# Kernel optimization log

Hardware: AMD Instinct MI355X
Metric: run time of the kernel (lower is better)

The kernel has to match this reference:

```python
import jax, jax.numpy as jnp
import numpy as np

THRESHOLD = 0.5
EPS = 1e-6


def setup_inputs() -> dict:
    key = jax.random.key(0)
    k1, k2 = jax.random.split(key)
    points = jax.random.normal(k1, (16, 10, 30, 2), dtype=jnp.float32)
    polys = jax.random.normal(k2, (16, 16, 200, 2), dtype=jnp.float32)
    return {"points": points, "drivable_multipolygon": polys}


def reference(points, drivable_multipolygon):
    # points: (B, C, T, 2); drivable_multipolygon: (B, K, N, 2)
    # Broadcast layout: (B, K, C, T, N-1, ...)
    ps = drivable_multipolygon[:, :, None, None, :-1, :]   # edge starts (B,K,1,1,N-1,2)
    pe = drivable_multipolygon[:, :, None, None, 1:, :]    # edge ends   (B,K,1,1,N-1,2)
    pts = points[:, None, :, :, None, :]                   # (B,1,C,T,1,2)

    # --- point-to-segment distance ---
    v1 = pts - ps
    ev = pe - ps
    dot = jnp.sum(v1 * ev, axis=-1)
    esq = jnp.sum(ev * ev, axis=-1)
    proj = jnp.clip(dot / (esq + EPS), 0.0, 1.0)
    closest = ev * proj[..., None] + ps
    dist_sq = jnp.maximum(jnp.sum((pts - closest) ** 2, axis=-1), EPS)
    min_dist = jnp.min(jnp.sqrt(dist_sq), axis=-1)         # min over edges N-1 -> (B,K,C,T)
    min_dist = jnp.min(min_dist, axis=1)                   # min over polygons K -> (B,C,T)

    # --- ray-casting inside test (parity of crossings) ---
    py = pts[..., 1]
    px = pts[..., 0]
    sy, sx = ps[..., 1], ps[..., 0]
    ey, ex = pe[..., 1], pe[..., 0]
    cond_y = ((sy <= py) & (py < ey)) | ((ey <= py) & (py < sy))
    slope = (ey - sy) / (ex - sx + EPS)
    intersect_x = sx + (py - sy) / (slope + EPS)
    is_left = intersect_x > px
    intersection = cond_y & is_left                        # (B,K,C,T,N-1)
    crossings = jnp.sum(jnp.sum(intersection.astype(jnp.int32), axis=-1), axis=1)  # (B,C,T)
    inside = (crossings % 2) == 1

    min_dist = jnp.where(inside, -min_dist, min_dist)
    min_dist = jax.nn.relu(min_dist + THRESHOLD)
    return jnp.sum(min_dist, axis=-1)                      # (B, C)
```

## Files before the change

kernel.cpp:

```cpp
#include <hip/hip_runtime.h>
#include <math.h>
#include <float.h>

#define EPS 1e-6f
#define THRESHOLD 0.5f

#define NB 16
#define NPOLY 16
#define NVERT 200
#define NSEG_PER_POLY 199
#define NSEG (NPOLY * NSEG_PER_POLY)
#define NPTB 300
#define HPTB 150
#define NPOINTS 4800
#define NSLICE 64
#define SEG_PER_SLICE 50


struct Seg { float sx, sy, evx, evy, inv_esq, errS, inv_slope, ey; };

__global__ __launch_bounds__(192) void seg_kernel(
    const float* __restrict__ points,
    const float* __restrict__ polys,
    float2* __restrict__ part,
    float* __restrict__ out)
{
    __shared__ float4 lds[SEG_PER_SLICE * 2];

    const int slice = blockIdx.x;
    const int b     = blockIdx.y;
    const int lp    = threadIdx.x;

    const int s0 = slice * SEG_PER_SLICE;
    const int s1 = (s0 + SEG_PER_SLICE < NSEG) ? s0 + SEG_PER_SLICE : NSEG;
    const int nseg = s1 - s0;

    const int p0i = b * NPTB + (lp < HPTB ? lp : 0);
    const float2 pt0 = ((const float2*)points)[p0i];
    const float2 pt1 = ((const float2*)points)[p0i + HPTB];

    if (lp < nseg) {
        const int s = s0 + lp;
        const int m = s / NSEG_PER_POLY;
        const int v = s % NSEG_PER_POLY;
        const float2* poly = (const float2*)polys + ((size_t)(b * NPOLY + m) * NVERT);
        const float2 S = poly[v];
        const float2 E = poly[v + 1];
        const float evx = E.x - S.x;
        const float evy = E.y - S.y;
        const float esq = evx * evx + evy * evy;
        const float inv_esq = 1.0f / (esq + EPS);
        const float slope_eps = evy / (evx + EPS) + EPS;
        const float inv_slope = __builtin_amdgcn_rcpf(slope_eps);
        const float errS = fmaf(fabsf(S.x), 1e-6f, 1e-30f);
        lds[lp * 2]     = make_float4(S.x, S.y, evx, evy);
        lds[lp * 2 + 1] = make_float4(inv_esq, errS, inv_slope, E.y);
    }
    __syncthreads();

    const float px0 = pt0.x, py0 = pt0.y;
    const float px1 = pt1.x, py1 = pt1.y;

    float mnA0 = FLT_MAX, mnB0 = FLT_MAX, mnA1 = FLT_MAX, mnB1 = FLT_MAX;
    int   crA0 = 0,       crB0 = 0,       crA1 = 0,       crB1 = 0;

    auto body = [&](const Seg& g, float px, float py, float& mn, int& cr) {
        const float v1x = px - g.sx;
        const float v1y = py - g.sy;
        const float dot = fmaf(v1y, g.evy, v1x * g.evx);
        const float t   = __builtin_amdgcn_fmed3f(dot * g.inv_esq, 0.0f, 1.0f);
        const float dx  = fmaf(-g.evx, t, v1x);
        const float dy  = fmaf(-g.evy, t, v1y);
        mn = fminf(mn, fmaf(dy, dy, dx * dx));

        const bool cond_y = (g.sy <= py) != (g.ey <= py);
        const float q    = v1y * g.inv_slope;
        const float diff = q - v1x;
        const float err  = fmaf(fabsf(q), 2e-6f, g.errS);
        bool left = diff > 0.0f;
        if (cond_y && !(fabsf(diff) > err)) {
            const float se = g.evy / (g.evx + EPS) + EPS;
            left = (g.sx + v1y / se) > px;
        }
        cr += (cond_y && left) ? 1 : 0;
    };

    auto ldseg = [&](int j) {
        const float4 a = lds[j * 2];
        const float4 c = lds[j * 2 + 1];
        return Seg{a.x, a.y, a.z, a.w, c.x, c.y, c.z, c.w};
    };

    for (int j = 0; j < nseg; j += 2) {
        const Seg gA = ldseg(j);
        const Seg gB = ldseg(j + 1);
        body(gA, px0, py0, mnA0, crA0);
        body(gA, px1, py1, mnA1, crA1);
        body(gB, px0, py0, mnB0, crB0);
        body(gB, px1, py1, mnB1, crB1);
    }

    if (lp < HPTB) {
        part[slice * NPOINTS + p0i] =
            make_float2(fminf(mnA0, mnB0), __int_as_float(crA0 + crB0));
        part[slice * NPOINTS + p0i + HPTB] =
            make_float2(fminf(mnA1, mnB1), __int_as_float(crA1 + crB1));
    } else if (slice == 0 && lp < HPTB + 10) {
        out[b * 10 + (lp - HPTB)] = 0.0f;
    }
}

__global__ __launch_bounds__(256) void final_kernel(
    const float2* __restrict__ part,
    float* __restrict__ out)
{
    const int p = blockIdx.x * 256 + threadIdx.x;
    if (p >= NPOINTS) return;

    float md = FLT_MAX;
    int c = 0;
    #pragma unroll 16
    for (int k = 0; k < NSLICE; ++k) {
        const float2 pr = part[k * NPOINTS + p];
        md = fminf(md, pr.x);
        c += __float_as_int(pr.y);
    }

    float d = sqrtf(fmaxf(md, EPS));
    if (c & 1) d = -d;
    const float val = fmaxf(d + THRESHOLD, 0.0f);

    const int b = p / NPTB;
    const int a = (p % NPTB) / 30;
    atomicAdd(out + b * 10 + a, val);
}

extern "C" void kernel_launch(void* const* d_in, const int* in_sizes, int n_in,
                              void* d_out, int out_size, void* d_ws, size_t ws_size,
                              hipStream_t stream) {
    const float* points = (const float*)d_in[0];
    const float* polys  = (const float*)d_in[1];
    float* out = (float*)d_out;

    float2* part = (float2*)d_ws;

    dim3 grid(NSLICE, NB);
    seg_kernel<<<grid, 192, 0, stream>>>(points, polys, part, out);
    final_kernel<<<(NPOINTS + 255) / 256, 256, 0, stream>>>(part, out);
}
```

Measured before the change: 80.71 us.

## Fuse segment and final kernels into one per-agent kernel with in-block reductions

Replaces the two-kernel scheme (segment slices writing partials to workspace, then a reduction kernel with atomics) with a single kernel per (batch, agent). Each 512-thread block holds 8 points per thread in registers and strides over all segments, computing segment data directly from global memory instead of staging it in LDS. Results are reduced with wave shuffles and shared memory, and the per-agent sum is written without atomics. This removes the second launch and the workspace round trip, but the grid shrinks to 160 blocks, and segment preprocessing is repeated per block and per point group.

```diff
diff --git a/kernel.cpp b/kernel.cpp
--- a/kernel.cpp
+++ b/kernel.cpp
@@ -10,129 +10,110 @@
 #define NVERT 200
 #define NSEG_PER_POLY 199
 #define NSEG (NPOLY * NSEG_PER_POLY)
-#define NPTB 300
-#define HPTB 150
-#define NPOINTS 4800
-#define NSLICE 64
-#define SEG_PER_SLICE 50
+#define NAGENT 10
+#define NPPA 30
+#define NPTB (NAGENT * NPPA)
+#define NTHREADS 512
+#define NCHUNK 128
+#define PSLOT 8
 
-
-struct Seg { float sx, sy, evx, evy, inv_esq, errS, inv_slope, ey; };
-
-__global__ __launch_bounds__(192) void seg_kernel(
+__global__ __launch_bounds__(NTHREADS) void fused_kernel(
     const float* __restrict__ points,
     const float* __restrict__ polys,
-    float2* __restrict__ part,
     float* __restrict__ out)
 {
-    __shared__ float4 lds[SEG_PER_SLICE * 2];
+    __shared__ float redmin[8][PSLOT];
+    __shared__ int   redcnt[8][PSLOT];
+    __shared__ float vals[NPPA];
 
-    const int slice = blockIdx.x;
+    const int agent = blockIdx.x;
     const int b     = blockIdx.y;
-    const int lp    = threadIdx.x;
+    const int t     = threadIdx.x;
+    const int sc    = t & (NCHUNK - 1);
+    const int pg    = t >> 7;
+    const int wv    = t >> 6;
+    const int lane  = t & 63;
 
-    const int s0 = slice * SEG_PER_SLICE;
-    const int s1 = (s0 + SEG_PER_SLICE < NSEG) ? s0 + SEG_PER_SLICE : NSEG;
-    const int nseg = s1 - s0;
+    float px[PSLOT], py[PSLOT], mins[PSLOT];
+    int   cnts[PSLOT];
+    const float2* pbase = (const float2*)points + ((size_t)b * NPTB + agent * NPPA);
+    #pragma unroll
+    for (int k = 0; k < PSLOT; ++k) {
+        int j = pg * PSLOT + k;
+        if (j > NPPA - 1) j = NPPA - 1;
+        const float2 p = pbase[j];
+        px[k] = p.x;  py[k] = p.y;
+        mins[k] = FLT_MAX;  cnts[k] = 0;
+    }
 
-    const int p0i = b * NPTB + (lp < HPTB ? lp : 0);
-    const float2 pt0 = ((const float2*)points)[p0i];
-    const float2 pt1 = ((const float2*)points)[p0i + HPTB];
+    const float2* pol = (const float2*)polys + (size_t)b * NPOLY * NVERT;
 
-    if (lp < nseg) {
-        const int s = s0 + lp;
-        const int m = s / NSEG_PER_POLY;
-        const int v = s % NSEG_PER_POLY;
-        const float2* poly = (const float2*)polys + ((size_t)(b * NPOLY + m) * NVERT);
-        const float2 S = poly[v];
-        const float2 E = poly[v + 1];
-        const float evx = E.x - S.x;
-        const float evy = E.y - S.y;
-        const float esq = evx * evx + evy * evy;
-        const float inv_esq = 1.0f / (esq + EPS);
+    for (int s = sc; s < NSEG; s += NCHUNK) {
+        const int m    = s / NSEG_PER_POLY;
+        const int v    = s - m * NSEG_PER_POLY;
+        const int base = m * NVERT + v;
+        const float2 S = pol[base];
+        const float2 E = pol[base + 1];
+        const float sx  = S.x, sy = S.y, ey = E.y;
+        const float evx = E.x - sx;
+        const float evy = ey - sy;
+        const float esq = fmaf(evx, evx, evy * evy);
+        const float inv_esq   = 1.0f / (esq + EPS);
         const float slope_eps = evy / (evx + EPS) + EPS;
         const float inv_slope = __builtin_amdgcn_rcpf(slope_eps);
-        const float errS = fmaf(fabsf(S.x), 1e-6f, 1e-30f);
-        lds[lp * 2]     = make_float4(S.x, S.y, evx, evy);
-        lds[lp * 2 + 1] = make_float4(inv_esq, errS, inv_slope, E.y);
+        const float errS      = fmaf(fabsf(sx), 1e-6f, 1e-30f);
+
+        #pragma unroll
+        for (int k = 0; k < PSLOT; ++k) {
+            const float v1x = px[k] - sx;
+            const float v1y = py[k] - sy;
+            const float dot = fmaf(v1y, evy, v1x * evx);
+            const float tt  = __builtin_amdgcn_fmed3f(dot * inv_esq, 0.0f, 1.0f);
+            const float dx  = fmaf(-evx, tt, v1x);
+            const float dy  = fmaf(-evy, tt, v1y);
+            mins[k] = fminf(mins[k], fmaf(dy, dy, dx * dx));
+
+            const bool  cond_y = (sy <= py[k]) != (ey <= py[k]);
+            const float q    = v1y * inv_slope;
+            const float diff = q - v1x;
+            const float err  = fmaf(fabsf(q), 2e-6f, errS);
+            bool left = diff > 0.0f;
+            if (cond_y && !(fabsf(diff) > err)) {
+                left = (sx + v1y / slope_eps) > px[k];
+            }
+            cnts[k] += (cond_y && left) ? 1 : 0;
+        }
+    }
+
+    #pragma unroll
+    for (int k = 0; k < PSLOT; ++k) {
+        float mn = mins[k];
+        int   cc = cnts[k];
+        #pragma unroll
+        for (int d = 1; d < 64; d <<= 1) {
+            mn = fminf(mn, __shfl_xor(mn, d, 64));
+            cc += __shfl_xor(cc, d, 64);
+        }
+        if (lane == 0) { redmin[wv][k] = mn; redcnt[wv][k] = cc; }
     }
     __syncthreads();
 
-    const float px0 = pt0.x, py0 = pt0.y;
-    const float px1 = pt1.x, py1 = pt1.y;
+    if (t < NPPA) {
+        const int jpg = t >> 3, k = t & 7;
+        const float mn = fminf(redmin[2 * jpg][k], redmin[2 * jpg + 1][k]);
+        const int   cc = redcnt[2 * jpg][k] + redcnt[2 * jpg + 1][k];
+        float d = sqrtf(fmaxf(mn, EPS));
+        if (cc & 1) d = -d;
+        vals[t] = fmaxf(d + THRESHOLD, 0.0f);
+    }
+    __syncthreads();
 
-    float mnA0 = FLT_MAX, mnB0 = FLT_MAX, mnA1 = FLT_MAX, mnB1 = FLT_MAX;
-    int   crA0 = 0,       crB0 = 0,       crA1 = 0,       crB1 = 0;
-
-    auto body = [&](const Seg& g, float px, float py, float& mn, int& cr) {
-        const float v1x = px - g.sx;
-        const float v1y = py - g.sy;
-        const float dot = fmaf(v1y, g.evy, v1x * g.evx);
-        const float t   = __builtin_amdgcn_fmed3f(dot * g.inv_esq, 0.0f, 1.0f);
-        const float dx  = fmaf(-g.evx, t, v1x);
-        const float dy  = fmaf(-g.evy, t, v1y);
-        mn = fminf(mn, fmaf(dy, dy, dx * dx));
-
-        const bool cond_y = (g.sy <= py) != (g.ey <= py);
-        const float q    = v1y * g.inv_slope;
-        const float diff = q - v1x;
-        const float err  = fmaf(fabsf(q), 2e-6f, g.errS);
-        bool left = diff > 0.0f;
-        if (cond_y && !(fabsf(diff) > err)) {
-            const float se = g.evy / (g.evx + EPS) + EPS;
-            left = (g.sx + v1y / se) > px;
-        }
-        cr += (cond_y && left) ? 1 : 0;
-    };
-
-    auto ldseg = [&](int j) {
-        const float4 a = lds[j * 2];
-        const float4 c = lds[j * 2 + 1];
-        return Seg{a.x, a.y, a.z, a.w, c.x, c.y, c.z, c.w};
-    };
-
-    for (int j = 0; j < nseg; j += 2) {
-        const Seg gA = ldseg(j);
-        const Seg gB = ldseg(j + 1);
-        body(gA, px0, py0, mnA0, crA0);
-        body(gA, px1, py1, mnA1, crA1);
-        body(gB, px0, py0, mnB0, crB0);
-        body(gB, px1, py1, mnB1, crB1);
+    if (t == 0) {
+        float ssum = 0.0f;
+        #pragma unroll
+        for (int j = 0; j < NPPA; ++j) ssum += vals[j];
+        out[b * NAGENT + agent] = ssum;
     }
-
-    if (lp < HPTB) {
-        part[slice * NPOINTS + p0i] =
-            make_float2(fminf(mnA0, mnB0), __int_as_float(crA0 + crB0));
-        part[slice * NPOINTS + p0i + HPTB] =
-            make_float2(fminf(mnA1, mnB1), __int_as_float(crA1 + crB1));
-    } else if (slice == 0 && lp < HPTB + 10) {
-        out[b * 10 + (lp - HPTB)] = 0.0f;
-    }
-}
-
-__global__ __launch_bounds__(256) void final_kernel(
-    const float2* __restrict__ part,
-    float* __restrict__ out)
-{
-    const int p = blockIdx.x * 256 + threadIdx.x;
-    if (p >= NPOINTS) return;
-
-    float md = FLT_MAX;
-    int c = 0;
-    #pragma unroll 16
-    for (int k = 0; k < NSLICE; ++k) {
-        const float2 pr = part[k * NPOINTS + p];
-        md = fminf(md, pr.x);
-        c += __float_as_int(pr.y);
-    }
-
-    float d = sqrtf(fmaxf(md, EPS));
-    if (c & 1) d = -d;
-    const float val = fmaxf(d + THRESHOLD, 0.0f);
-
-    const int b = p / NPTB;
-    const int a = (p % NPTB) / 30;
-    atomicAdd(out + b * 10 + a, val);
 }
 
 extern "C" void kernel_launch(void* const* d_in, const int* in_sizes, int n_in,
@@ -142,9 +123,8 @@
     const float* polys  = (const float*)d_in[1];
     float* out = (float*)d_out;
 
-    float2* part = (float2*)d_ws;
+    (void)d_ws; (void)ws_size;
 
-    dim3 grid(NSLICE, NB);
-    seg_kernel<<<grid, 192, 0, stream>>>(points, polys, part, out);
-    final_kernel<<<(NPOINTS + 255) / 256, 256, 0, stream>>>(part, out);
+    dim3 grid(NAGENT, NB);
+    fused_kernel<<<grid, NTHREADS, 0, stream>>>(points, polys, out);
 }
```

Result: no change. 80.79 us (+0.1%).
